# Kernel tuning notes

Hardware: AMD Instinct MI355X
Metric: run time of the kernel (lower is better)

Reference implementation:

```python
import jax, jax.numpy as jnp
import numpy as np

MODES = 256


def setup_inputs() -> dict:
    key = jax.random.key(0)
    k1, k2, k3, k4, k5 = jax.random.split(key, 5)
    B, C_IN, C_OUT, N, KM = 8, 128, 128, 8192, 32
    scale = 1.0 / (C_IN * C_OUT)
    return {
        "x": jax.random.normal(k1, (B, C_IN, N), dtype=jnp.float32),
        "wbases": jax.random.normal(k2, (B, N, MODES), dtype=jnp.float32),
        "bases": jax.random.normal(k3, (B, N, MODES), dtype=jnp.float32),
        "weights": scale * jax.random.normal(k4, (C_IN, C_OUT, KM), dtype=jnp.float32),
        "D": jax.random.normal(k5, (KM, MODES), dtype=jnp.float32),
    }


def reference(x, wbases, bases, weights, D):
    # Project onto weighted bases: (b, c_in, n) x (b, n, modes) -> (b, c_in, modes)
    x_hat = jnp.einsum('bcx,bxk->bck', x, wbases[:, :, :MODES])
    # D-weighted channel mixing. Original: x_hat1[b,i,j,k] = x_hat[b,i,k]*D[j,k];
    # y[b,o,k] = sum_{i,j} x_hat1[b,i,j,k] * weights[i,o,j]
    # Equivalent fused contraction (same math, no 4D broadcast):
    y_hat = jnp.einsum('bik,jk,ioj->bok', x_hat, D, weights)
    # Reconstruct on output bases: (b, c_out, modes) x (b, n, modes) -> (b, c_out, n)
    y = jnp.einsum('bck,bxk->bcx', y_hat, bases[:, :, :MODES])
    return y
```

## Files before the change

kernel.cpp:

```cpp
#include <hip/hip_runtime.h>

#define B_    8
#define CIN   128
#define COUT  128
#define NX    8192
#define KMJ   32
#define MODES 256

typedef short bf16x8 __attribute__((ext_vector_type(8)));
typedef float f32x4  __attribute__((ext_vector_type(4)));

__device__ __forceinline__ float bf2f(unsigned short u) {
    union { unsigned int i; float f; } v; v.i = ((unsigned int)u) << 16; return v.f;
}
__device__ __forceinline__ unsigned short f2bf(float f) {
    union { float f; unsigned int i; } v; v.f = f;
    unsigned int x = v.i;
    return (unsigned short)((x + 0x7fffu + ((x >> 16) & 1u)) >> 16);
}
__device__ __forceinline__ bf16x8 cvt8(const float* __restrict__ p) {
    f32x4 a = *(const f32x4*)p;
    f32x4 b = *(const f32x4*)(p + 4);
    bf16x8 r;
    r[0] = (short)f2bf(a[0]); r[1] = (short)f2bf(a[1]);
    r[2] = (short)f2bf(a[2]); r[3] = (short)f2bf(a[3]);
    r[4] = (short)f2bf(b[0]); r[5] = (short)f2bf(b[1]);
    r[6] = (short)f2bf(b[2]); r[7] = (short)f2bf(b[3]);
    return r;
}
__device__ __forceinline__ ushort4 cvt4(f32x4 a) {
    ushort4 r;
    r.x = f2bf(a[0]); r.y = f2bf(a[1]); r.z = f2bf(a[2]); r.w = f2bf(a[3]);
    return r;
}

__global__ __launch_bounds__(256) void k1_wk(const float* __restrict__ W,
                                             const float* __restrict__ D,
                                             unsigned short* __restrict__ Wk) {
    int wave = threadIdx.x >> 6, lane = threadIdx.x & 63;
    int quad = lane >> 4, l16 = lane & 15;
    int gw  = blockIdx.x * 4 + wave;
    int oi0 = gw * 16;
    int i0  = oi0 & 127, o0 = oi0 >> 7;
    bf16x8 bfrag = cvt8(W + ((size_t)(i0 + l16) * COUT + o0) * KMJ + quad * 8);
    for (int mt = 0; mt < 16; mt++) {
        int k0 = mt * 16;
        bf16x8 afrag;
#pragma unroll
        for (int jj = 0; jj < 8; jj++)
            afrag[jj] = (short)f2bf(D[(quad * 8 + jj) * MODES + k0 + l16]);
        f32x4 acc = {0.f, 0.f, 0.f, 0.f};
        acc = __builtin_amdgcn_mfma_f32_16x16x32_bf16(afrag, bfrag, acc, 0, 0, 0);
#pragma unroll
        for (int r = 0; r < 4; r++)
            Wk[(size_t)(k0 + quad * 4 + r) * (CIN * COUT) + oi0 + l16] = f2bf(acc[r]);
    }
}

__global__ __launch_bounds__(256) void k2_xhat(const float* __restrict__ X,
                                               const float* __restrict__ WB,
                                               unsigned short* __restrict__ PART) {
    __shared__ __align__(16) unsigned short Xs[128 * 40];
    __shared__ __align__(16) unsigned short WBs[32 * 68];
    int nt = blockIdx.x, kt = blockIdx.y, b = blockIdx.z;
    int r0 = nt * 256;
    int t  = threadIdx.x;
    int wave = t >> 6, lane = t & 63;
    int wm = wave >> 1, wn = wave & 1;
    int quad = lane >> 4, l16 = lane & 15;

    const float* xb  = X  + (size_t)b * CIN * NX;
    const float* wbb = WB + (size_t)b * NX * MODES + kt * 64;

    int xn4 = t & 7,  xc  = t >> 3;
    int wk4 = t & 15, wn0 = t >> 4;

    f32x4 acc[4][2];
#pragma unroll
    for (int i = 0; i < 4; i++)
#pragma unroll
        for (int j = 0; j < 2; j++) acc[i][j] = (f32x4){0.f, 0.f, 0.f, 0.f};

    for (int s = 0; s < 8; s++) {
        int rs = r0 + s * 32;
        f32x4 xv[4], wv[2];
#pragma unroll
        for (int r = 0; r < 4; r++)
            xv[r] = *(const f32x4*)(xb + (size_t)(xc + 32 * r) * NX + rs + xn4 * 4);
#pragma unroll
        for (int r = 0; r < 2; r++)
            wv[r] = *(const f32x4*)(wbb + (size_t)(rs + wn0 + 16 * r) * MODES + wk4 * 4);

        __syncthreads();
#pragma unroll
        for (int r = 0; r < 4; r++)
            *(ushort4*)(Xs + (xc + 32 * r) * 40 + xn4 * 4) = cvt4(xv[r]);
#pragma unroll
        for (int r = 0; r < 2; r++)
            *(ushort4*)(WBs + (wn0 + 16 * r) * 68 + wk4 * 4) = cvt4(wv[r]);
        __syncthreads();

        bf16x8 af[4];
#pragma unroll
        for (int tm = 0; tm < 4; tm++)
            af[tm] = *(const bf16x8*)(Xs + (wm * 64 + tm * 16 + l16) * 40 + quad * 8);
        bf16x8 bfv[2];
#pragma unroll
        for (int tn = 0; tn < 2; tn++) {
            int km = wn * 32 + tn * 16 + l16;
#pragma unroll
            for (int jj = 0; jj < 8; jj++)
                bfv[tn][jj] = (short)WBs[(quad * 8 + jj) * 68 + km];
        }
#pragma unroll
        for (int tm = 0; tm < 4; tm++)
#pragma unroll
            for (int tn = 0; tn < 2; tn++)
                acc[tm][tn] = __builtin_amdgcn_mfma_f32_16x16x32_bf16(af[tm], bfv[tn], acc[tm][tn], 0, 0, 0);
    }

    unsigned short* pb = PART + ((size_t)b * 32 + nt) * (CIN * MODES) + kt * 64;
#pragma unroll
    for (int tm = 0; tm < 4; tm++) {
        int c = wm * 64 + tm * 16 + quad * 4;
#pragma unroll
        for (int tn = 0; tn < 2; tn++) {
            int km = wn * 32 + tn * 16 + l16;
#pragma unroll
            for (int r = 0; r < 4; r++)
                pb[(size_t)(c + r) * MODES + km] = f2bf(acc[tm][tn][r]);
        }
    }
}

__global__ __launch_bounds__(256) void k2b_red(const unsigned short* __restrict__ PART,
                                               float* __restrict__ XH) {
    int e0 = blockIdx.x * 1024 + threadIdx.x;
#pragma unroll
    for (int r = 0; r < 4; r++) {
        int e = e0 + r * 256;
        int b = e >> 15, rem = e & 32767;
        const unsigned short* p = PART + (size_t)b * 32 * (CIN * MODES) + rem;
        float acc = 0.f;
#pragma unroll
        for (int nt = 0; nt < 32; nt++) acc += bf2f(p[nt * (CIN * MODES)]);
        XH[e] = acc;
    }
}

__global__ __launch_bounds__(256) void k3_yhat(const float* __restrict__ XH,
                                               const unsigned short* __restrict__ Wk,
                                               unsigned short* __restrict__ YH) {
    __shared__ float xs[128][8];
    int k = blockIdx.x, oc = blockIdx.y;
    int t = threadIdx.x;
#pragma unroll
    for (int l = 0; l < 4; l++) {
        int e = l * 256 + t;
        int i = e >> 3, b = e & 7;
        xs[i][b] = XH[(size_t)b * (CIN * MODES) + (size_t)i * MODES + k];
    }
    __syncthreads();
    int o = oc * 32 + (t >> 3), b = t & 7;
    const unsigned short* wp = Wk + (size_t)k * (CIN * COUT) + (size_t)o * CIN;
    float acc = 0.f;
#pragma unroll 4
    for (int ii = 0; ii < 16; ii++) {
        bf16x8 wc = *(const bf16x8*)(wp + ii * 8);
#pragma unroll
        for (int jj = 0; jj < 8; jj++)
            acc += bf2f((unsigned short)wc[jj]) * xs[ii * 8 + jj][b];
    }
    YH[((size_t)b * COUT + o) * MODES + k] = f2bf(acc);
}

__global__ __launch_bounds__(256) void k4_y(const unsigned short* __restrict__ YH,
                                            const float* __restrict__ BA,
                                            float* __restrict__ Y) {
    __shared__ __align__(16) unsigned short As[128 * 36];
    __shared__ __align__(16) unsigned short Bs[64 * 36];
    int nt = blockIdx.x, b = blockIdx.y;
    int n0 = nt * 64;
    int t  = threadIdx.x;
    int wave = t >> 6, lane = t & 63;
    int wm = wave >> 1, wn = wave & 1;
    int quad = lane >> 4, l16 = lane & 15;

    const unsigned short* yhb = YH + (size_t)b * COUT * MODES;
    const float* bab = BA + (size_t)b * NX * MODES + (size_t)n0 * MODES;

    int E0  = t * 8;
    int ar0 = E0 >> 5, akk = E0 & 31;
    int ar1 = (2048 + E0) >> 5;
    int bk4 = t & 7, bn = t >> 3;

    f32x4 acc[4][2];
#pragma unroll
    for (int i = 0; i < 4; i++)
#pragma unroll
        for (int j = 0; j < 2; j++) acc[i][j] = (f32x4){0.f, 0.f, 0.f, 0.f};

    for (int step = 0; step < 8; step++) {
        int ks = step * 32;
        bf16x8 av0 = *(const bf16x8*)(yhb + (size_t)ar0 * MODES + ks + akk);
        bf16x8 av1 = *(const bf16x8*)(yhb + (size_t)ar1 * MODES + ks + akk);
        f32x4 bv[2];
#pragma unroll
        for (int r = 0; r < 2; r++)
            bv[r] = *(const f32x4*)(bab + (size_t)(bn + 32 * r) * MODES + ks + bk4 * 4);

        __syncthreads();
        *(bf16x8*)(As + ar0 * 36 + akk) = av0;
        *(bf16x8*)(As + ar1 * 36 + akk) = av1;
#pragma unroll
        for (int r = 0; r < 2; r++)
            *(ushort4*)(Bs + (bn + 32 * r) * 36 + bk4 * 4) = cvt4(bv[r]);
        __syncthreads();

        bf16x8 af[4], bfv[2];
#pragma unroll
        for (int tm = 0; tm < 4; tm++)
            af[tm] = *(const bf16x8*)(As + (wm * 64 + tm * 16 + l16) * 36 + quad * 8);
#pragma unroll
        for (int tn = 0; tn < 2; tn++)
            bfv[tn] = *(const bf16x8*)(Bs + (wn * 32 + tn * 16 + l16) * 36 + quad * 8);
#pragma unroll
        for (int tm = 0; tm < 4; tm++)
#pragma unroll
            for (int tn = 0; tn < 2; tn++)
                acc[tm][tn] = __builtin_amdgcn_mfma_f32_16x16x32_bf16(af[tm], bfv[tn], acc[tm][tn], 0, 0, 0);
    }

    float* yb = Y + (size_t)b * COUT * NX;
#pragma unroll
    for (int tm = 0; tm < 4; tm++) {
        int o = wm * 64 + tm * 16 + quad * 4;
#pragma unroll
        for (int tn = 0; tn < 2; tn++) {
            int n = n0 + wn * 32 + tn * 16 + l16;
#pragma unroll
            for (int r = 0; r < 4; r++)
                yb[(size_t)(o + r) * NX + n] = acc[tm][tn][r];
        }
    }
}

extern "C" void kernel_launch(void* const* d_in, const int* in_sizes, int n_in,
                              void* d_out, int out_size, void* d_ws, size_t ws_size,
                              hipStream_t stream) {
    const float* X  = (const float*)d_in[0];
    const float* WB = (const float*)d_in[1];
    const float* BA = (const float*)d_in[2];
    const float* W  = (const float*)d_in[3];
    const float* D  = (const float*)d_in[4];
    float* Y = (float*)d_out;

    char* ws = (char*)d_ws;
    unsigned short* Wk   = (unsigned short*)ws;
    float*          XH   = (float*)(ws + (8u << 20));
    unsigned short* YH   = (unsigned short*)(ws + (9u << 20));
    unsigned short* PART = (unsigned short*)(ws + (10u << 20));

    k1_wk  <<<256,             256, 0, stream>>>(W, D, Wk);
    k2_xhat<<<dim3(32, 4, 8),  256, 0, stream>>>(X, WB, PART);
    k2b_red<<<256,             256, 0, stream>>>(PART, XH);
    k3_yhat<<<dim3(256, 4),    256, 0, stream>>>(XH, Wk, YH);
    k4_y   <<<dim3(128, 8),    256, 0, stream>>>(YH, BA, Y);
}
```

Before: 232.6 us.

## Retile all stages with larger blocks, double-buffered LDS and transposed basis staging

k1 is split across four mode groups for more blocks. k2 now covers all 256 modes per block with 512 threads, so each x tile is read once rather than four times. The bases are stored transposed into LDS for vectorized fragment loads, and LDS is double-buffered so each step needs one barrier instead of two. k4 prefetches the next global tile into registers, uses 128-wide n tiles with double-buffered LDS, and k3 uses four independent accumulators. In exchange, k2 produces twice as many n-partials, which doubles the partial-sum buffer and the reduction traffic.

```diff
diff --git a/kernel.cpp b/kernel.cpp
--- a/kernel.cpp
+++ b/kernel.cpp
@@ -43,8 +43,9 @@
     int oi0 = gw * 16;
     int i0  = oi0 & 127, o0 = oi0 >> 7;
     bf16x8 bfrag = cvt8(W + ((size_t)(i0 + l16) * COUT + o0) * KMJ + quad * 8);
-    for (int mt = 0; mt < 16; mt++) {
-        int k0 = mt * 16;
+#pragma unroll
+    for (int mtl = 0; mtl < 4; mtl++) {
+        int k0 = (blockIdx.y * 4 + mtl) * 16;
         bf16x8 afrag;
 #pragma unroll
         for (int jj = 0; jj < 8; jj++)
@@ -57,75 +58,71 @@
     }
 }
 
-__global__ __launch_bounds__(256) void k2_xhat(const float* __restrict__ X,
-                                               const float* __restrict__ WB,
-                                               unsigned short* __restrict__ PART) {
-    __shared__ __align__(16) unsigned short Xs[128 * 40];
-    __shared__ __align__(16) unsigned short WBs[32 * 68];
-    int nt = blockIdx.x, kt = blockIdx.y, b = blockIdx.z;
-    int r0 = nt * 256;
+__global__ __launch_bounds__(512, 4) void k2_xhat(const float* __restrict__ X,
+                                                  const float* __restrict__ WB,
+                                                  unsigned short* __restrict__ PART) {
+    __shared__ __align__(16) unsigned short Xs[2][128 * 40];
+    __shared__ __align__(16) unsigned short WBT[2][256 * 34];
+    int nt = blockIdx.x, b = blockIdx.y;
+    int r0 = nt * 128;
     int t  = threadIdx.x;
     int wave = t >> 6, lane = t & 63;
-    int wm = wave >> 1, wn = wave & 1;
+    int wm = wave >> 2, wn = wave & 3;
     int quad = lane >> 4, l16 = lane & 15;
 
     const float* xb  = X  + (size_t)b * CIN * NX;
-    const float* wbb = WB + (size_t)b * NX * MODES + kt * 64;
+    const float* wbb = WB + (size_t)b * NX * MODES;
 
     int xn4 = t & 7,  xc  = t >> 3;
-    int wk4 = t & 15, wn0 = t >> 4;
-
-    f32x4 acc[4][2];
+    int wk4 = t & 63, wn0 = t >> 6;
+
+    f32x4 acc[4][4];
 #pragma unroll
     for (int i = 0; i < 4; i++)
 #pragma unroll
-        for (int j = 0; j < 2; j++) acc[i][j] = (f32x4){0.f, 0.f, 0.f, 0.f};
-
-    for (int s = 0; s < 8; s++) {
-        int rs = r0 + s * 32;
-        f32x4 xv[4], wv[2];
+        for (int j = 0; j < 4; j++) acc[i][j] = (f32x4){0.f, 0.f, 0.f, 0.f};
+
+    for (int s = 0; s < 4; s++) {
+        int ns = r0 + s * 32;
+        int bs = s & 1;
+        f32x4 xv0 = *(const f32x4*)(xb + (size_t)xc * NX + ns + xn4 * 4);
+        f32x4 xv1 = *(const f32x4*)(xb + (size_t)(xc + 64) * NX + ns + xn4 * 4);
+        f32x4 wv[4];
 #pragma unroll
         for (int r = 0; r < 4; r++)
-            xv[r] = *(const f32x4*)(xb + (size_t)(xc + 32 * r) * NX + rs + xn4 * 4);
-#pragma unroll
-        for (int r = 0; r < 2; r++)
-            wv[r] = *(const f32x4*)(wbb + (size_t)(rs + wn0 + 16 * r) * MODES + wk4 * 4);
-
+            wv[r] = *(const f32x4*)(wbb + (size_t)(ns + wn0 + 8 * r) * MODES + wk4 * 4);
+
+        *(ushort4*)(Xs[bs] + xc * 40 + xn4 * 4)        = cvt4(xv0);
+        *(ushort4*)(Xs[bs] + (xc + 64) * 40 + xn4 * 4) = cvt4(xv1);
+#pragma unroll
+        for (int r = 0; r < 4; r++)
+#pragma unroll
+            for (int q = 0; q < 4; q++)
+                WBT[bs][(wk4 * 4 + q) * 34 + wn0 + 8 * r] = f2bf(wv[r][q]);
         __syncthreads();
-#pragma unroll
-        for (int r = 0; r < 4; r++)
-            *(ushort4*)(Xs + (xc + 32 * r) * 40 + xn4 * 4) = cvt4(xv[r]);
-#pragma unroll
-        for (int r = 0; r < 2; r++)
-            *(ushort4*)(WBs + (wn0 + 16 * r) * 68 + wk4 * 4) = cvt4(wv[r]);
-        __syncthreads();
 
         bf16x8 af[4];
 #pragma unroll
         for (int tm = 0; tm < 4; tm++)
-            af[tm] = *(const bf16x8*)(Xs + (wm * 64 + tm * 16 + l16) * 40 + quad * 8);
-        bf16x8 bfv[2];
-#pragma unroll
-        for (int tn = 0; tn < 2; tn++) {
-            int km = wn * 32 + tn * 16 + l16;
-#pragma unroll
-            for (int jj = 0; jj < 8; jj++)
-                bfv[tn][jj] = (short)WBs[(quad * 8 + jj) * 68 + km];
-        }
-#pragma unroll
-        for (int tm = 0; tm < 4; tm++)
-#pragma unroll
-            for (int tn = 0; tn < 2; tn++)
+            af[tm] = *(const bf16x8*)(Xs[bs] + (wm * 64 + tm * 16 + l16) * 40 + quad * 8);
+        bf16x8 bfv[4];
+#pragma unroll
+        for (int tn = 0; tn < 4; tn++)
+            bfv[tn] = *(const bf16x8*)(WBT[bs] + (wn * 64 + tn * 16 + l16) * 34 + quad * 8);
+#pragma unroll
+        for (int tm = 0; tm < 4; tm++)
+#pragma unroll
+            for (int tn = 0; tn < 4; tn++)
                 acc[tm][tn] = __builtin_amdgcn_mfma_f32_16x16x32_bf16(af[tm], bfv[tn], acc[tm][tn], 0, 0, 0);
     }
 
-    unsigned short* pb = PART + ((size_t)b * 32 + nt) * (CIN * MODES) + kt * 64;
+    unsigned short* pb = PART + ((size_t)b * 64 + nt) * (CIN * MODES);
 #pragma unroll
     for (int tm = 0; tm < 4; tm++) {
         int c = wm * 64 + tm * 16 + quad * 4;
 #pragma unroll
-        for (int tn = 0; tn < 2; tn++) {
-            int km = wn * 32 + tn * 16 + l16;
+        for (int tn = 0; tn < 4; tn++) {
+            int km = wn * 64 + tn * 16 + l16;
 #pragma unroll
             for (int r = 0; r < 4; r++)
                 pb[(size_t)(c + r) * MODES + km] = f2bf(acc[tm][tn][r]);
@@ -135,15 +132,15 @@
 
 __global__ __launch_bounds__(256) void k2b_red(const unsigned short* __restrict__ PART,
                                                float* __restrict__ XH) {
-    int e0 = blockIdx.x * 1024 + threadIdx.x;
-#pragma unroll
-    for (int r = 0; r < 4; r++) {
+    int e0 = blockIdx.x * 512 + threadIdx.x;
+#pragma unroll
+    for (int r = 0; r < 2; r++) {
         int e = e0 + r * 256;
         int b = e >> 15, rem = e & 32767;
-        const unsigned short* p = PART + (size_t)b * 32 * (CIN * MODES) + rem;
+        const unsigned short* p = PART + (size_t)b * 64 * (CIN * MODES) + rem;
         float acc = 0.f;
 #pragma unroll
-        for (int nt = 0; nt < 32; nt++) acc += bf2f(p[nt * (CIN * MODES)]);
+        for (int nt = 0; nt < 64; nt++) acc += bf2f(p[nt * (CIN * MODES)]);
         XH[e] = acc;
     }
 }
@@ -163,36 +160,39 @@
     __syncthreads();
     int o = oc * 32 + (t >> 3), b = t & 7;
     const unsigned short* wp = Wk + (size_t)k * (CIN * COUT) + (size_t)o * CIN;
-    float acc = 0.f;
-#pragma unroll 4
+    float a0 = 0.f, a1 = 0.f, a2 = 0.f, a3 = 0.f;
+#pragma unroll
     for (int ii = 0; ii < 16; ii++) {
         bf16x8 wc = *(const bf16x8*)(wp + ii * 8);
-#pragma unroll
-        for (int jj = 0; jj < 8; jj++)
-            acc += bf2f((unsigned short)wc[jj]) * xs[ii * 8 + jj][b];
-    }
-    YH[((size_t)b * COUT + o) * MODES + k] = f2bf(acc);
-}
-
-__global__ __launch_bounds__(256) void k4_y(const unsigned short* __restrict__ YH,
-                                            const float* __restrict__ BA,
-                                            float* __restrict__ Y) {
-    __shared__ __align__(16) unsigned short As[128 * 36];
-    __shared__ __align__(16) unsigned short Bs[64 * 36];
+        a0 += bf2f((unsigned short)wc[0]) * xs[ii * 8 + 0][b];
+        a1 += bf2f((unsigned short)wc[1]) * xs[ii * 8 + 1][b];
+        a2 += bf2f((unsigned short)wc[2]) * xs[ii * 8 + 2][b];
+        a3 += bf2f((unsigned short)wc[3]) * xs[ii * 8 + 3][b];
+        a0 += bf2f((unsigned short)wc[4]) * xs[ii * 8 + 4][b];
+        a1 += bf2f((unsigned short)wc[5]) * xs[ii * 8 + 5][b];
+        a2 += bf2f((unsigned short)wc[6]) * xs[ii * 8 + 6][b];
+        a3 += bf2f((unsigned short)wc[7]) * xs[ii * 8 + 7][b];
+    }
+    YH[((size_t)b * COUT + o) * MODES + k] = f2bf((a0 + a1) + (a2 + a3));
+}
+
+__global__ __launch_bounds__(512, 4) void k4_y(const unsigned short* __restrict__ YH,
+                                               const float* __restrict__ BA,
+                                               float* __restrict__ Y) {
+    __shared__ __align__(16) unsigned short As[2][128 * 36];
+    __shared__ __align__(16) unsigned short Bs[2][128 * 36];
     int nt = blockIdx.x, b = blockIdx.y;
-    int n0 = nt * 64;
+    int n0 = nt * 128;
     int t  = threadIdx.x;
     int wave = t >> 6, lane = t & 63;
-    int wm = wave >> 1, wn = wave & 1;
+    int wm = wave >> 2, wn = wave & 3;
     int quad = lane >> 4, l16 = lane & 15;
 
     const unsigned short* yhb = YH + (size_t)b * COUT * MODES;
     const float* bab = BA + (size_t)b * NX * MODES + (size_t)n0 * MODES;
 
-    int E0  = t * 8;
-    int ar0 = E0 >> 5, akk = E0 & 31;
-    int ar1 = (2048 + E0) >> 5;
-    int bk4 = t & 7, bn = t >> 3;
+    int ar  = t >> 2, akk = (t & 3) * 8;
+    int bk4 = t & 7,  bn  = t >> 3;
 
     f32x4 acc[4][2];
 #pragma unroll
@@ -200,30 +200,31 @@
 #pragma unroll
         for (int j = 0; j < 2; j++) acc[i][j] = (f32x4){0.f, 0.f, 0.f, 0.f};
 
-    for (int step = 0; step < 8; step++) {
-        int ks = step * 32;
-        bf16x8 av0 = *(const bf16x8*)(yhb + (size_t)ar0 * MODES + ks + akk);
-        bf16x8 av1 = *(const bf16x8*)(yhb + (size_t)ar1 * MODES + ks + akk);
-        f32x4 bv[2];
-#pragma unroll
-        for (int r = 0; r < 2; r++)
-            bv[r] = *(const f32x4*)(bab + (size_t)(bn + 32 * r) * MODES + ks + bk4 * 4);
-
+    bf16x8 av  = *(const bf16x8*)(yhb + (size_t)ar * MODES + akk);
+    f32x4  bv0 = *(const f32x4*)(bab + (size_t)bn * MODES + bk4 * 4);
+    f32x4  bv1 = *(const f32x4*)(bab + (size_t)(bn + 64) * MODES + bk4 * 4);
+
+    for (int s = 0; s < 8; s++) {
+        int bs = s & 1;
+        *(bf16x8*)(As[bs] + ar * 36 + akk)          = av;
+        *(ushort4*)(Bs[bs] + bn * 36 + bk4 * 4)        = cvt4(bv0);
+        *(ushort4*)(Bs[bs] + (bn + 64) * 36 + bk4 * 4) = cvt4(bv1);
         __syncthreads();
-        *(bf16x8*)(As + ar0 * 36 + akk) = av0;
-        *(bf16x8*)(As + ar1 * 36 + akk) = av1;
-#pragma unroll
-        for (int r = 0; r < 2; r++)
-            *(ushort4*)(Bs + (bn + 32 * r) * 36 + bk4 * 4) = cvt4(bv[r]);
-        __syncthreads();
+
+        if (s < 7) {
+            int ks = (s + 1) * 32;
+            av  = *(const bf16x8*)(yhb + (size_t)ar * MODES + ks + akk);
+            bv0 = *(const f32x4*)(bab + (size_t)bn * MODES + ks + bk4 * 4);
+            bv1 = *(const f32x4*)(bab + (size_t)(bn + 64) * MODES + ks + bk4 * 4);
+        }
 
         bf16x8 af[4], bfv[2];
 #pragma unroll
         for (int tm = 0; tm < 4; tm++)
-            af[tm] = *(const bf16x8*)(As + (wm * 64 + tm * 16 + l16) * 36 + quad * 8);
+            af[tm] = *(const bf16x8*)(As[bs] + (wm * 64 + tm * 16 + l16) * 36 + quad * 8);
 #pragma unroll
         for (int tn = 0; tn < 2; tn++)
-            bfv[tn] = *(const bf16x8*)(Bs + (wn * 32 + tn * 16 + l16) * 36 + quad * 8);
+            bfv[tn] = *(const bf16x8*)(Bs[bs] + (wn * 32 + tn * 16 + l16) * 36 + quad * 8);
 #pragma unroll
         for (int tm = 0; tm < 4; tm++)
 #pragma unroll
@@ -234,13 +235,13 @@
     float* yb = Y + (size_t)b * COUT * NX;
 #pragma unroll
     for (int tm = 0; tm < 4; tm++) {
-        int o = wm * 64 + tm * 16 + quad * 4;
+        int c = wm * 64 + tm * 16 + quad * 4;
 #pragma unroll
         for (int tn = 0; tn < 2; tn++) {
             int n = n0 + wn * 32 + tn * 16 + l16;
 #pragma unroll
             for (int r = 0; r < 4; r++)
-                yb[(size_t)(o + r) * NX + n] = acc[tm][tn][r];
+                yb[(size_t)(c + r) * NX + n] = acc[tm][tn][r];
         }
     }
 }
@@ -256,14 +257,14 @@
     float* Y = (float*)d_out;
 
     char* ws = (char*)d_ws;
-    unsigned short* Wk   = (unsigned short*)ws;
-    float*          XH   = (float*)(ws + (8u << 20));
-    unsigned short* YH   = (unsigned short*)(ws + (9u << 20));
-    unsigned short* PART = (unsigned short*)(ws + (10u << 20));
-
-    k1_wk  <<<256,             256, 0, stream>>>(W, D, Wk);
-    k2_xhat<<<dim3(32, 4, 8),  256, 0, stream>>>(X, WB, PART);
-    k2b_red<<<256,             256, 0, stream>>>(PART, XH);
-    k3_yhat<<<dim3(256, 4),    256, 0, stream>>>(XH, Wk, YH);
-    k4_y   <<<dim3(128, 8),    256, 0, stream>>>(YH, BA, Y);
-}
+    unsigned short* PART = (unsigned short*)ws;
+    unsigned short* Wk   = (unsigned short*)(ws + (34u << 20));
+    float*          XH   = (float*)(ws + (42u << 20));
+    unsigned short* YH   = (unsigned short*)(ws + (43u << 20));
+
+    k1_wk  <<<dim3(256, 4),   256, 0, stream>>>(W, D, Wk);
+    k2_xhat<<<dim3(64, 8),    512, 0, stream>>>(X, WB, PART);
+    k2b_red<<<512,            256, 0, stream>>>(PART, XH);
+    k3_yhat<<<dim3(256, 4),   256, 0, stream>>>(XH, Wk, YH);
+    k4_y   <<<dim3(64, 8),    512, 0, stream>>>(YH, BA, Y);
+}
```

After: 228.5 us. Within noise of the previous version (-1.8%).
